# Performance work log

Hardware: AMD Instinct MI355X
Metric: run time of the kernel (lower is better)

## Reference

```python
import jax, jax.numpy as jnp
import numpy as np

B, L, D = 4, 128, 256
EPS = 1e-5

def setup_inputs() -> dict:
    key = jax.random.key(0)
    k1, k2, k3, k4, k5 = jax.random.split(key, 5)
    query = jax.random.normal(k1, (B, L, D), dtype=jnp.float32)
    value = jax.random.normal(k2, (B, L, D), dtype=jnp.float32)
    mask = jax.random.randint(k3, (B, L), 0, 2, dtype=jnp.int32)
    mask = mask.at[:, 0].set(1)  # guarantee at least one valid key per row (avoid all -inf softmax)
    norm3_w = jax.random.normal(k4, (2 * D,), dtype=jnp.float32) * 0.02 + 1.0
    norm3_b = jax.random.normal(k5, (2 * D,), dtype=jnp.float32) * 0.02
    return {"query": query, "value": value, "mask": mask, "norm3_w": norm3_w, "norm3_b": norm3_b}

def reference(query, value, mask, norm3_w, norm3_b):
    # final_queryer[b,i,j,d] = (query[b,i,d] + value[b,j,d]) / 2  -- replaces the eye-matrix expansion
    fq = (query[:, :, None, :] + value[:, None, :, :]) * 0.5          # [B,L,L,D]
    # scores over key axis k against value / query banks
    w = jnp.einsum('bijd,bkd->bijk', fq, value)                        # [B,L,L,L]
    wq = jnp.einsum('bijd,bkd->bijk', fq, query)                       # [B,L,L,L]
    keymask = (mask == 0)[:, None, None, :]                            # [B,1,1,L]
    neg_inf = jnp.float32(-jnp.inf)
    w = jnp.where(keymask, neg_inf, w)
    wq = jnp.where(keymask, neg_inf, wq)
    attn = jax.nn.softmax(w, axis=3)
    attn_q = jax.nn.softmax(wq, axis=3)
    merged = jnp.einsum('bijk,bkd->bijd', attn, value)                 # [B,L,L,D]
    merged_q = jnp.einsum('bijk,bkd->bijd', attn_q, query)             # [B,L,L,D]
    merged = jnp.concatenate([merged, merged_q], axis=-1)              # [B,L,L,2D]
    # LayerNorm over last dim (2D)
    mu = jnp.mean(merged, axis=-1, keepdims=True)
    var = jnp.mean((merged - mu) ** 2, axis=-1, keepdims=True)
    merged = (merged - mu) * jax.lax.rsqrt(var + EPS) * norm3_w + norm3_b
    # re-mask along the i axis
    merged = merged * mask[:, :, None, None].astype(merged.dtype)
    return merged
```

## Files before the change

### kernel.cpp

```cpp
#include <hip/hip_runtime.h>
#include <hip/hip_bf16.h>
#include <stdint.h>

#define BDIM 4
#define LDIM 128
#define DDIM 256
#define CDIM 512
#define EPSLN 1e-5f
#define NE (BDIM * LDIM * LDIM)
#define SROW 516

typedef float f32x4 __attribute__((ext_vector_type(4)));
typedef short s16x8 __attribute__((ext_vector_type(8)));
typedef int i32x4 __attribute__((ext_vector_type(4)));

__device__ __forceinline__ unsigned short f2bf(float f) {
    unsigned u = __builtin_bit_cast(unsigned, f);
    u += 0x7fffu + ((u >> 16) & 1u);
    return (unsigned short)(u >> 16);
}

__device__ __forceinline__ unsigned pk_bf16(float a, float b) {
    union { __hip_bfloat162 h; unsigned u; } cv;
    cv.h = __float22bfloat162_rn(make_float2(a, b));
    return cv.u;
}

__global__ __launch_bounds__(256) void k_transpose(const float* __restrict__ query,
                                                   const float* __restrict__ value,
                                                   float* __restrict__ Qt32,
                                                   float* __restrict__ Vt32,
                                                   unsigned short* __restrict__ Qt16,
                                                   unsigned short* __restrict__ Vt16) {
    __shared__ float tile[32][33];
    const int d0 = blockIdx.x * 32, k0 = blockIdx.y * 32;
    const int b = blockIdx.z & 3, sel = blockIdx.z >> 2;
    const float* src = sel ? query : value;
    float* dst32 = sel ? Qt32 : Vt32;
    unsigned short* dst16 = sel ? Qt16 : Vt16;
    const int tx = threadIdx.x & 31, ty = threadIdx.x >> 5;
#pragma unroll
    for (int jj = 0; jj < 4; ++jj) {
        int r = ty + jj * 8;
        tile[r][tx] = src[((size_t)(b * LDIM + k0 + r)) * DDIM + d0 + tx];
    }
    __syncthreads();
#pragma unroll
    for (int jj = 0; jj < 4; ++jj) {
        int r = ty + jj * 8;
        float v = tile[tx][r];
        size_t o = ((size_t)(b * DDIM + d0 + r)) * LDIM + k0 + tx;
        dst32[o] = v;
        dst16[o] = f2bf(v);
    }
}

__global__ __launch_bounds__(128) void k_gram_e(const float* __restrict__ Qt,
                                                const float* __restrict__ Vt,
                                                const int* __restrict__ mask,
                                                float* __restrict__ Es) {
    const int it = blockIdx.x, which = blockIdx.y, b = blockIdx.z;
    const float* Xt;
    const float* Yt;
    if (which == 0)      { Xt = Qt; Yt = Vt; }
    else if (which == 1) { Xt = Vt; Yt = Vt; }
    else if (which == 2) { Xt = Qt; Yt = Qt; }
    else                 { Xt = Vt; Yt = Qt; }

    const int i0 = it * 16 + ((threadIdx.x >> 5) << 2);
    const int kt = (threadIdx.x & 31) << 2;
    const float* xb = Xt + (size_t)b * DDIM * LDIM + i0;
    const float* yb = Yt + (size_t)b * DDIM * LDIM + kt;

    float acc[4][4] = {};
#pragma unroll 8
    for (int c = 0; c < DDIM; ++c) {
        f32x4 xv = *(const f32x4*)(xb + (size_t)c * LDIM);
        f32x4 yv = *(const f32x4*)(yb + (size_t)c * LDIM);
#pragma unroll
        for (int ii = 0; ii < 4; ++ii)
#pragma unroll
            for (int kk = 0; kk < 4; ++kk)
                acc[ii][kk] += xv[ii] * yv[kk];
    }

    const i32x4 mv = *(const i32x4*)(mask + b * LDIM + kt);
    float* Eg = Es + (size_t)which * NE + (size_t)b * (LDIM * LDIM);
#pragma unroll
    for (int ii = 0; ii < 4; ++ii) {
        float lg[4];
        float mx = -3.0e38f;
#pragma unroll
        for (int kk = 0; kk < 4; ++kk) {
            lg[kk] = 0.5f * acc[ii][kk];
            if (mv[kk] != 0) mx = fmaxf(mx, lg[kk]);
        }
#pragma unroll
        for (int o = 16; o >= 1; o >>= 1) mx = fmaxf(mx, __shfl_xor(mx, o, 64));
        f32x4 r;
#pragma unroll
        for (int kk = 0; kk < 4; ++kk) r[kk] = (mv[kk] != 0) ? __expf(lg[kk] - mx) : 0.0f;
        *(f32x4*)(Eg + (size_t)(i0 + ii) * LDIM + kt) = r;
    }
}

__global__ __launch_bounds__(256, 2) void k_main(const float* __restrict__ E1,
                                                 const unsigned short* __restrict__ Vt16,
                                                 const unsigned short* __restrict__ Qt16,
                                                 const int* __restrict__ mask,
                                                 const float* __restrict__ nw,
                                                 const float* __restrict__ nb,
                                                 float* __restrict__ out) {
    __shared__ __align__(16) char smem[32 * SROW * 4];
    unsigned short (*P_s)[136] = (unsigned short (*)[136])smem;
    unsigned short (*Pq_s)[136] = (unsigned short (*)[136])(smem + 32 * 136 * 2);
    float (*stage)[SROW] = (float (*)[SROW])smem;
    __shared__ float wln[CDIM], bln[CDIM];
    __shared__ float zinv_s[64];
    __shared__ float maskv[32];

    const int tid = threadIdx.x;
    const int i0 = blockIdx.x * 32;
    const int j = blockIdx.y;
    const int b = blockIdx.z;

    const int lane = tid & 63;
    const int q = lane >> 4;
    const int l15 = lane & 15;
    const int wv = tid >> 6;
    const int path = wv >> 1;
    const int nh = wv & 1;

    const float* E2 = E1 + NE;
    const float* E1q = E1 + 2 * NE;
    const float* E2q = E1 + 3 * NE;

    wln[tid] = nw[tid]; wln[tid + 256] = nw[tid + 256];
    bln[tid] = nb[tid]; bln[tid + 256] = nb[tid + 256];
    if (tid < 32) maskv[tid] = (mask[b * LDIM + i0 + tid] != 0) ? 1.0f : 0.0f;

    const unsigned short* bsrc = (path ? Qt16 : Vt16) +
                                 (size_t)b * DDIM * LDIM + (size_t)(nh * 128) * LDIM;
    s16x8 bfr[8][4];
#pragma unroll
    for (int nt = 0; nt < 8; ++nt)
#pragma unroll
        for (int kc = 0; kc < 4; ++kc)
            bfr[nt][kc] = *(const s16x8*)(bsrc + (size_t)(nt * 16 + l15) * LDIM + kc * 32 + q * 8);

    {
        const int m = tid >> 3;
        const int k0 = (tid & 7) * 16;
        const float* e1 = E1 + ((size_t)(b * LDIM + i0 + m)) * LDIM + k0;
        const float* e1q = E1q + ((size_t)(b * LDIM + i0 + m)) * LDIM + k0;
        const float* e2 = E2 + ((size_t)(b * LDIM + j)) * LDIM + k0;
        const float* e2q = E2q + ((size_t)(b * LDIM + j)) * LDIM + k0;
        union { unsigned u32[8]; s16x8 v[2]; } tp, tq;
        float s = 0.f, sq = 0.f;
#pragma unroll
        for (int u4 = 0; u4 < 16; u4 += 4) {
            f32x4 a = *(const f32x4*)(e1 + u4);
            f32x4 c = *(const f32x4*)(e2 + u4);
            f32x4 aq = *(const f32x4*)(e1q + u4);
            f32x4 cq = *(const f32x4*)(e2q + u4);
            float p0 = a[0] * c[0], p1 = a[1] * c[1], p2 = a[2] * c[2], p3 = a[3] * c[3];
            float q0 = aq[0] * cq[0], q1 = aq[1] * cq[1], q2 = aq[2] * cq[2], q3 = aq[3] * cq[3];
            s += (p0 + p1) + (p2 + p3);
            sq += (q0 + q1) + (q2 + q3);
            tp.u32[u4 / 2] = pk_bf16(p0, p1);
            tp.u32[u4 / 2 + 1] = pk_bf16(p2, p3);
            tq.u32[u4 / 2] = pk_bf16(q0, q1);
            tq.u32[u4 / 2 + 1] = pk_bf16(q2, q3);
        }
        *(s16x8*)&P_s[m][k0] = tp.v[0];
        *(s16x8*)&P_s[m][k0 + 8] = tp.v[1];
        *(s16x8*)&Pq_s[m][k0] = tq.v[0];
        *(s16x8*)&Pq_s[m][k0 + 8] = tq.v[1];
        s += __shfl_xor(s, 1, 64); s += __shfl_xor(s, 2, 64); s += __shfl_xor(s, 4, 64);
        sq += __shfl_xor(sq, 1, 64); sq += __shfl_xor(sq, 2, 64); sq += __shfl_xor(sq, 4, 64);
        if ((tid & 7) == 0) { zinv_s[m] = 1.0f / s; zinv_s[32 + m] = 1.0f / sq; }
    }
    __syncthreads();

    f32x4 acc[2][8];
#pragma unroll
    for (int mt = 0; mt < 2; ++mt)
#pragma unroll
        for (int nt = 0; nt < 8; ++nt) acc[mt][nt] = (f32x4){0.f, 0.f, 0.f, 0.f};

    const unsigned short(*As)[136] = path ? Pq_s : P_s;
#pragma unroll
    for (int kc = 0; kc < 4; ++kc) {
        const s16x8 a0 = *(const s16x8*)&As[l15][kc * 32 + q * 8];
        const s16x8 a1 = *(const s16x8*)&As[16 + l15][kc * 32 + q * 8];
#pragma unroll
        for (int nt = 0; nt < 8; ++nt) {
            acc[0][nt] = __builtin_amdgcn_mfma_f32_16x16x32_bf16(a0, bfr[nt][kc], acc[0][nt], 0, 0, 0);
            acc[1][nt] = __builtin_amdgcn_mfma_f32_16x16x32_bf16(a1, bfr[nt][kc], acc[1][nt], 0, 0, 0);
        }
    }
    __syncthreads();

#pragma unroll
    for (int mt = 0; mt < 2; ++mt) {
#pragma unroll
        for (int reg = 0; reg < 4; ++reg) {
            const int row = mt * 16 + q * 4 + reg;
            const float zv = zinv_s[path * 32 + row];
#pragma unroll
            for (int nt = 0; nt < 8; ++nt) {
                const int c = path * 256 + nh * 128 + nt * 16 + l15;
                stage[row][c] = acc[mt][nt][reg] * zv;
            }
        }
    }
    __syncthreads();

    {
        const f32x4 w0 = *(const f32x4*)&wln[lane * 4];
        const f32x4 b0 = *(const f32x4*)&bln[lane * 4];
        const f32x4 w1 = *(const f32x4*)&wln[256 + lane * 4];
        const f32x4 b1 = *(const f32x4*)&bln[256 + lane * 4];
#pragma unroll
        for (int rr = 0; rr < 8; ++rr) {
            const int row = wv * 8 + rr;
            const f32x4 v0 = *(const f32x4*)&stage[row][lane * 4];
            const f32x4 v1 = *(const f32x4*)&stage[row][256 + lane * 4];
            float s1 = (v0[0] + v0[1]) + (v0[2] + v0[3]) + (v1[0] + v1[1]) + (v1[2] + v1[3]);
            float s2 = (v0[0] * v0[0] + v0[1] * v0[1]) + (v0[2] * v0[2] + v0[3] * v0[3]) +
                       (v1[0] * v1[0] + v1[1] * v1[1]) + (v1[2] * v1[2] + v1[3] * v1[3]);
#pragma unroll
            for (int o = 1; o <= 32; o <<= 1) {
                s1 += __shfl_xor(s1, o, 64);
                s2 += __shfl_xor(s2, o, 64);
            }
            const float mean = s1 * (1.0f / 512.0f);
            const float var = s2 * (1.0f / 512.0f) - mean * mean;
            const float rstd = rsqrtf(var + EPSLN);
            const float mf = maskv[row];
            float* orow = out + (((size_t)(b * LDIM + i0 + row)) * LDIM + j) * CDIM;
            f32x4 o0, o1;
#pragma unroll
            for (int u = 0; u < 4; ++u) {
                o0[u] = ((v0[u] - mean) * rstd * w0[u] + b0[u]) * mf;
                o1[u] = ((v1[u] - mean) * rstd * w1[u] + b1[u]) * mf;
            }
            *(f32x4*)&orow[lane * 4] = o0;
            *(f32x4*)&orow[256 + lane * 4] = o1;
        }
    }
}

extern "C" void kernel_launch(void* const* d_in, const int* in_sizes, int n_in,
                              void* d_out, int out_size, void* d_ws, size_t ws_size,
                              hipStream_t stream) {
    const float* query = (const float*)d_in[0];
    const float* value = (const float*)d_in[1];
    const int* mask = (const int*)d_in[2];
    const float* nw = (const float*)d_in[3];
    const float* nb = (const float*)d_in[4];
    float* out = (float*)d_out;

    char* ws = (char*)d_ws;
    const size_t NT = (size_t)BDIM * DDIM * LDIM;

    float* Es = (float*)ws;
    unsigned short* Vt16 = (unsigned short*)(ws + 4 * (size_t)NE * 4);
    unsigned short* Qt16 = Vt16 + NT;
    float* Vt32 = (float*)(ws + 4 * (size_t)NE * 4 + 2 * NT * 2);
    float* Qt32 = Vt32 + NT;

    k_transpose<<<dim3(8, 4, 8), 256, 0, stream>>>(query, value, Qt32, Vt32, Qt16, Vt16);
    k_gram_e<<<dim3(8, 4, 4), 128, 0, stream>>>(Qt32, Vt32, mask, Es);
    k_main<<<dim3(4, 128, 4), 256, 0, stream>>>(Es, Vt16, Qt16, mask, nw, nb, out);
}
```

Baseline: 238.3 us.

## Process four j per block and fuse LayerNorm into MFMA registers

Each k_main block now handles four j values instead of one. This amortizes the B-fragment register loads, the LN weight loads and the E1 row loads across four outputs, and cuts the grid size by four. The LayerNorm no longer stages the full 32x512 tile in shared memory. Row sums are reduced directly from the MFMA accumulators with shuffles plus a small double-buffered cross-wave buffer, and outputs are written straight from registers. The trade-off is that output stores become scalar strided writes (16 lanes contiguous) instead of 128-bit vector stores, and there is less block-level parallelism.

```diff
diff --git a/kernel.cpp b/kernel.cpp
--- a/kernel.cpp
+++ b/kernel.cpp
@@ -8,7 +8,7 @@
 #define CDIM 512
 #define EPSLN 1e-5f
 #define NE (BDIM * LDIM * LDIM)
-#define SROW 516
+#define JT 4
 
 typedef float f32x4 __attribute__((ext_vector_type(4)));
 typedef short s16x8 __attribute__((ext_vector_type(8)));
@@ -111,17 +111,15 @@
                                                  const float* __restrict__ nw,
                                                  const float* __restrict__ nb,
                                                  float* __restrict__ out) {
-    __shared__ __align__(16) char smem[32 * SROW * 4];
-    unsigned short (*P_s)[136] = (unsigned short (*)[136])smem;
-    unsigned short (*Pq_s)[136] = (unsigned short (*)[136])(smem + 32 * 136 * 2);
-    float (*stage)[SROW] = (float (*)[SROW])smem;
+    __shared__ __align__(16) unsigned short P_s[JT][2][32][136];
     __shared__ float wln[CDIM], bln[CDIM];
-    __shared__ float zinv_s[64];
+    __shared__ float zinv_s[JT][2][32];
+    __shared__ __align__(16) float red[2][32][4][2];
     __shared__ float maskv[32];
 
     const int tid = threadIdx.x;
     const int i0 = blockIdx.x * 32;
-    const int j = blockIdx.y;
+    const int j0 = blockIdx.y * JT;
     const int b = blockIdx.z;
 
     const int lane = tid & 63;
@@ -153,101 +151,105 @@
         const int k0 = (tid & 7) * 16;
         const float* e1 = E1 + ((size_t)(b * LDIM + i0 + m)) * LDIM + k0;
         const float* e1q = E1q + ((size_t)(b * LDIM + i0 + m)) * LDIM + k0;
-        const float* e2 = E2 + ((size_t)(b * LDIM + j)) * LDIM + k0;
-        const float* e2q = E2q + ((size_t)(b * LDIM + j)) * LDIM + k0;
-        union { unsigned u32[8]; s16x8 v[2]; } tp, tq;
-        float s = 0.f, sq = 0.f;
+        const float* e2 = E2 + ((size_t)(b * LDIM + j0)) * LDIM + k0;
+        const float* e2q = E2q + ((size_t)(b * LDIM + j0)) * LDIM + k0;
+        float s[JT] = {}, sq[JT] = {};
 #pragma unroll
         for (int u4 = 0; u4 < 16; u4 += 4) {
-            f32x4 a = *(const f32x4*)(e1 + u4);
-            f32x4 c = *(const f32x4*)(e2 + u4);
-            f32x4 aq = *(const f32x4*)(e1q + u4);
-            f32x4 cq = *(const f32x4*)(e2q + u4);
-            float p0 = a[0] * c[0], p1 = a[1] * c[1], p2 = a[2] * c[2], p3 = a[3] * c[3];
-            float q0 = aq[0] * cq[0], q1 = aq[1] * cq[1], q2 = aq[2] * cq[2], q3 = aq[3] * cq[3];
-            s += (p0 + p1) + (p2 + p3);
-            sq += (q0 + q1) + (q2 + q3);
-            tp.u32[u4 / 2] = pk_bf16(p0, p1);
-            tp.u32[u4 / 2 + 1] = pk_bf16(p2, p3);
-            tq.u32[u4 / 2] = pk_bf16(q0, q1);
-            tq.u32[u4 / 2 + 1] = pk_bf16(q2, q3);
-        }
-        *(s16x8*)&P_s[m][k0] = tp.v[0];
-        *(s16x8*)&P_s[m][k0 + 8] = tp.v[1];
-        *(s16x8*)&Pq_s[m][k0] = tq.v[0];
-        *(s16x8*)&Pq_s[m][k0 + 8] = tq.v[1];
-        s += __shfl_xor(s, 1, 64); s += __shfl_xor(s, 2, 64); s += __shfl_xor(s, 4, 64);
-        sq += __shfl_xor(sq, 1, 64); sq += __shfl_xor(sq, 2, 64); sq += __shfl_xor(sq, 4, 64);
-        if ((tid & 7) == 0) { zinv_s[m] = 1.0f / s; zinv_s[32 + m] = 1.0f / sq; }
+            const f32x4 a = *(const f32x4*)(e1 + u4);
+            const f32x4 aq = *(const f32x4*)(e1q + u4);
+#pragma unroll
+            for (int jj = 0; jj < JT; ++jj) {
+                const f32x4 c = *(const f32x4*)(e2 + jj * LDIM + u4);
+                const f32x4 cq = *(const f32x4*)(e2q + jj * LDIM + u4);
+                const float p0 = a[0] * c[0], p1 = a[1] * c[1];
+                const float p2 = a[2] * c[2], p3 = a[3] * c[3];
+                const float r0 = aq[0] * cq[0], r1 = aq[1] * cq[1];
+                const float r2 = aq[2] * cq[2], r3 = aq[3] * cq[3];
+                s[jj] += (p0 + p1) + (p2 + p3);
+                sq[jj] += (r0 + r1) + (r2 + r3);
+                uint2 wp; wp.x = pk_bf16(p0, p1); wp.y = pk_bf16(p2, p3);
+                uint2 wq2; wq2.x = pk_bf16(r0, r1); wq2.y = pk_bf16(r2, r3);
+                *(uint2*)&P_s[jj][0][m][k0 + u4] = wp;
+                *(uint2*)&P_s[jj][1][m][k0 + u4] = wq2;
+            }
+        }
+#pragma unroll
+        for (int jj = 0; jj < JT; ++jj) {
+            float s_ = s[jj], sq_ = sq[jj];
+            s_ += __shfl_xor(s_, 1, 64); s_ += __shfl_xor(s_, 2, 64); s_ += __shfl_xor(s_, 4, 64);
+            sq_ += __shfl_xor(sq_, 1, 64); sq_ += __shfl_xor(sq_, 2, 64); sq_ += __shfl_xor(sq_, 4, 64);
+            if ((tid & 7) == 0) { zinv_s[jj][0][m] = 1.0f / s_; zinv_s[jj][1][m] = 1.0f / sq_; }
+        }
     }
     __syncthreads();
 
-    f32x4 acc[2][8];
-#pragma unroll
-    for (int mt = 0; mt < 2; ++mt)
-#pragma unroll
-        for (int nt = 0; nt < 8; ++nt) acc[mt][nt] = (f32x4){0.f, 0.f, 0.f, 0.f};
-
-    const unsigned short(*As)[136] = path ? Pq_s : P_s;
-#pragma unroll
-    for (int kc = 0; kc < 4; ++kc) {
-        const s16x8 a0 = *(const s16x8*)&As[l15][kc * 32 + q * 8];
-        const s16x8 a1 = *(const s16x8*)&As[16 + l15][kc * 32 + q * 8];
-#pragma unroll
-        for (int nt = 0; nt < 8; ++nt) {
-            acc[0][nt] = __builtin_amdgcn_mfma_f32_16x16x32_bf16(a0, bfr[nt][kc], acc[0][nt], 0, 0, 0);
-            acc[1][nt] = __builtin_amdgcn_mfma_f32_16x16x32_bf16(a1, bfr[nt][kc], acc[1][nt], 0, 0, 0);
-        }
-    }
-    __syncthreads();
-
-#pragma unroll
-    for (int mt = 0; mt < 2; ++mt) {
-#pragma unroll
-        for (int reg = 0; reg < 4; ++reg) {
-            const int row = mt * 16 + q * 4 + reg;
-            const float zv = zinv_s[path * 32 + row];
+    const int c0 = path * 256 + nh * 128 + l15;
+    float wreg[8], breg[8];
+#pragma unroll
+    for (int nt = 0; nt < 8; ++nt) { wreg[nt] = wln[c0 + nt * 16]; breg[nt] = bln[c0 + nt * 16]; }
+
+#pragma unroll 1
+    for (int jj = 0; jj < JT; ++jj) {
+        f32x4 acc[2][8];
+#pragma unroll
+        for (int mt = 0; mt < 2; ++mt)
+#pragma unroll
+            for (int nt = 0; nt < 8; ++nt) acc[mt][nt] = (f32x4){0.f, 0.f, 0.f, 0.f};
+
+        const unsigned short(*As)[136] = P_s[jj][path];
+#pragma unroll
+        for (int kc = 0; kc < 4; ++kc) {
+            const s16x8 a0 = *(const s16x8*)&As[l15][kc * 32 + q * 8];
+            const s16x8 a1 = *(const s16x8*)&As[16 + l15][kc * 32 + q * 8];
 #pragma unroll
             for (int nt = 0; nt < 8; ++nt) {
-                const int c = path * 256 + nh * 128 + nt * 16 + l15;
-                stage[row][c] = acc[mt][nt][reg] * zv;
-            }
-        }
-    }
-    __syncthreads();
-
-    {
-        const f32x4 w0 = *(const f32x4*)&wln[lane * 4];
-        const f32x4 b0 = *(const f32x4*)&bln[lane * 4];
-        const f32x4 w1 = *(const f32x4*)&wln[256 + lane * 4];
-        const f32x4 b1 = *(const f32x4*)&bln[256 + lane * 4];
-#pragma unroll
-        for (int rr = 0; rr < 8; ++rr) {
-            const int row = wv * 8 + rr;
-            const f32x4 v0 = *(const f32x4*)&stage[row][lane * 4];
-            const f32x4 v1 = *(const f32x4*)&stage[row][256 + lane * 4];
-            float s1 = (v0[0] + v0[1]) + (v0[2] + v0[3]) + (v1[0] + v1[1]) + (v1[2] + v1[3]);
-            float s2 = (v0[0] * v0[0] + v0[1] * v0[1]) + (v0[2] * v0[2] + v0[3] * v0[3]) +
-                       (v1[0] * v1[0] + v1[1] * v1[1]) + (v1[2] * v1[2] + v1[3] * v1[3]);
-#pragma unroll
-            for (int o = 1; o <= 32; o <<= 1) {
-                s1 += __shfl_xor(s1, o, 64);
-                s2 += __shfl_xor(s2, o, 64);
-            }
-            const float mean = s1 * (1.0f / 512.0f);
-            const float var = s2 * (1.0f / 512.0f) - mean * mean;
-            const float rstd = rsqrtf(var + EPSLN);
-            const float mf = maskv[row];
-            float* orow = out + (((size_t)(b * LDIM + i0 + row)) * LDIM + j) * CDIM;
-            f32x4 o0, o1;
-#pragma unroll
-            for (int u = 0; u < 4; ++u) {
-                o0[u] = ((v0[u] - mean) * rstd * w0[u] + b0[u]) * mf;
-                o1[u] = ((v1[u] - mean) * rstd * w1[u] + b1[u]) * mf;
-            }
-            *(f32x4*)&orow[lane * 4] = o0;
-            *(f32x4*)&orow[256 + lane * 4] = o1;
-        }
+                acc[0][nt] = __builtin_amdgcn_mfma_f32_16x16x32_bf16(a0, bfr[nt][kc], acc[0][nt], 0, 0, 0);
+                acc[1][nt] = __builtin_amdgcn_mfma_f32_16x16x32_bf16(a1, bfr[nt][kc], acc[1][nt], 0, 0, 0);
+            }
+        }
+
+        const int rb = jj & 1;
+#pragma unroll
+        for (int mt = 0; mt < 2; ++mt)
+#pragma unroll
+            for (int reg = 0; reg < 4; ++reg) {
+                const int row = mt * 16 + q * 4 + reg;
+                const float zv = zinv_s[jj][path][row];
+                float s1 = 0.f, s2 = 0.f;
+#pragma unroll
+                for (int nt = 0; nt < 8; ++nt) {
+                    const float v = acc[mt][nt][reg] * zv;
+                    acc[mt][nt][reg] = v;
+                    s1 += v; s2 += v * v;
+                }
+#pragma unroll
+                for (int o = 1; o <= 8; o <<= 1) {
+                    s1 += __shfl_xor(s1, o, 64);
+                    s2 += __shfl_xor(s2, o, 64);
+                }
+                if (l15 == 0) { red[rb][row][wv][0] = s1; red[rb][row][wv][1] = s2; }
+            }
+        __syncthreads();
+
+#pragma unroll
+        for (int mt = 0; mt < 2; ++mt)
+#pragma unroll
+            for (int reg = 0; reg < 4; ++reg) {
+                const int row = mt * 16 + q * 4 + reg;
+                const f32x4 r0 = *(const f32x4*)&red[rb][row][0][0];
+                const f32x4 r1 = *(const f32x4*)&red[rb][row][2][0];
+                const float s1t = (r0[0] + r0[2]) + (r1[0] + r1[2]);
+                const float s2t = (r0[1] + r0[3]) + (r1[1] + r1[3]);
+                const float mean = s1t * (1.0f / 512.0f);
+                const float var = s2t * (1.0f / 512.0f) - mean * mean;
+                const float rstd = rsqrtf(var + EPSLN);
+                const float mf = maskv[row];
+                float* orow = out + (((size_t)(b * LDIM + i0 + row)) * LDIM + (j0 + jj)) * CDIM + c0;
+#pragma unroll
+                for (int nt = 0; nt < 8; ++nt)
+                    orow[nt * 16] = ((acc[mt][nt][reg] - mean) * rstd * wreg[nt] + breg[nt]) * mf;
+            }
     }
 }
 
@@ -272,5 +274,5 @@
 
     k_transpose<<<dim3(8, 4, 8), 256, 0, stream>>>(query, value, Qt32, Vt32, Qt16, Vt16);
     k_gram_e<<<dim3(8, 4, 4), 128, 0, stream>>>(Qt32, Vt32, mask, Es);
-    k_main<<<dim3(4, 128, 4), 256, 0, stream>>>(Es, Vt16, Qt16, mask, nw, nb, out);
-}
+    k_main<<<dim3(4, 32, 4), 256, 0, stream>>>(Es, Vt16, Qt16, mask, nw, nb, out);
+}
```

Result: slower. 253.3 us (+6.3%).

## Fuse transpose and gram-softmax kernels into one prep kernel using LDS tiles

Applied to the files above, without the earlier changes.

Merges the transpose and Gram/exp kernels into a single launch. The Gram computation now reads query/value directly in row-major form, staged through shared memory, instead of going through fp32 transposed copies. This removes the fp32 transpose writes, one kernel launch, and a dependency stage. The cost is more shared memory per block and Es stores that are no longer vectorised.

```diff
diff --git a/kernel.cpp b/kernel.cpp
--- a/kernel.cpp
+++ b/kernel.cpp
@@ -26,65 +26,93 @@
     return cv.u;
 }
 
-__global__ __launch_bounds__(256) void k_transpose(const float* __restrict__ query,
-                                                   const float* __restrict__ value,
-                                                   float* __restrict__ Qt32,
-                                                   float* __restrict__ Vt32,
-                                                   unsigned short* __restrict__ Qt16,
-                                                   unsigned short* __restrict__ Vt16) {
-    __shared__ float tile[32][33];
-    const int d0 = blockIdx.x * 32, k0 = blockIdx.y * 32;
-    const int b = blockIdx.z & 3, sel = blockIdx.z >> 2;
-    const float* src = sel ? query : value;
-    float* dst32 = sel ? Qt32 : Vt32;
-    unsigned short* dst16 = sel ? Qt16 : Vt16;
-    const int tx = threadIdx.x & 31, ty = threadIdx.x >> 5;
-#pragma unroll
-    for (int jj = 0; jj < 4; ++jj) {
-        int r = ty + jj * 8;
-        tile[r][tx] = src[((size_t)(b * LDIM + k0 + r)) * DDIM + d0 + tx];
-    }
-    __syncthreads();
-#pragma unroll
-    for (int jj = 0; jj < 4; ++jj) {
-        int r = ty + jj * 8;
-        float v = tile[tx][r];
-        size_t o = ((size_t)(b * DDIM + d0 + r)) * LDIM + k0 + tx;
-        dst32[o] = v;
-        dst16[o] = f2bf(v);
-    }
-}
-
-__global__ __launch_bounds__(128) void k_gram_e(const float* __restrict__ Qt,
-                                                const float* __restrict__ Vt,
-                                                const int* __restrict__ mask,
-                                                float* __restrict__ Es) {
-    const int it = blockIdx.x, which = blockIdx.y, b = blockIdx.z;
-    const float* Xt;
-    const float* Yt;
-    if (which == 0)      { Xt = Qt; Yt = Vt; }
-    else if (which == 1) { Xt = Vt; Yt = Vt; }
-    else if (which == 2) { Xt = Qt; Yt = Qt; }
-    else                 { Xt = Vt; Yt = Qt; }
-
-    const int i0 = it * 16 + ((threadIdx.x >> 5) << 2);
-    const int kt = (threadIdx.x & 31) << 2;
-    const float* xb = Xt + (size_t)b * DDIM * LDIM + i0;
-    const float* yb = Yt + (size_t)b * DDIM * LDIM + kt;
+__global__ __launch_bounds__(128) void k_prep(const float* __restrict__ query,
+                                              const float* __restrict__ value,
+                                              const int* __restrict__ mask,
+                                              float* __restrict__ Es,
+                                              unsigned short* __restrict__ Qt16,
+                                              unsigned short* __restrict__ Vt16) {
+    __shared__ __align__(16) char smem[16 * 260 * 4 + 128 * 68 * 4];
+    float (*X_s)[260] = (float (*)[260])smem;
+    float (*Y_s)[68] = (float (*)[68])(smem + 16 * 260 * 4);
+    float (*tile)[33] = (float (*)[33])smem;
+
+    const int t = threadIdx.x;
+
+    if (blockIdx.z >= 4) {
+        const int z2 = blockIdx.z - 4;
+        const int b = z2 & 3, sel = z2 >> 2;
+        const int d0 = blockIdx.x * 32, k0 = blockIdx.y * 32;
+        const float* src = sel ? query : value;
+        unsigned short* dst16 = sel ? Qt16 : Vt16;
+        const int tx = t & 31, ty = t >> 5;
+#pragma unroll
+        for (int jj = 0; jj < 8; ++jj) {
+            int r = ty + jj * 4;
+            tile[r][tx] = src[((size_t)(b * LDIM + k0 + r)) * DDIM + d0 + tx];
+        }
+        __syncthreads();
+#pragma unroll
+        for (int jj = 0; jj < 8; ++jj) {
+            int r = ty + jj * 4;
+            size_t o = ((size_t)(b * DDIM + d0 + r)) * LDIM + k0 + tx;
+            dst16[o] = f2bf(tile[tx][r]);
+        }
+        return;
+    }
+
+    const int b = blockIdx.z, which = blockIdx.y, it = blockIdx.x;
+    const float* X = (which == 0 || which == 2) ? query : value;
+    const float* Y = (which <= 1) ? value : query;
+    const float* Xb = X + (size_t)b * LDIM * DDIM;
+    const float* Yb = Y + (size_t)b * LDIM * DDIM;
+
+    const int i0 = it * 16;
+    const int iq = (t >> 5) << 2;
+    const int kl = t & 31;
+
+#pragma unroll
+    for (int u = 0; u < 8; ++u) {
+        int ch = u * 128 + t;
+        int row = ch >> 6;
+        int cc = (ch & 63) << 2;
+        *(f32x4*)&X_s[row][cc] = *(const f32x4*)(Xb + (size_t)(i0 + row) * DDIM + cc);
+    }
 
     float acc[4][4] = {};
-#pragma unroll 8
-    for (int c = 0; c < DDIM; ++c) {
-        f32x4 xv = *(const f32x4*)(xb + (size_t)c * LDIM);
-        f32x4 yv = *(const f32x4*)(yb + (size_t)c * LDIM);
-#pragma unroll
-        for (int ii = 0; ii < 4; ++ii)
-#pragma unroll
-            for (int kk = 0; kk < 4; ++kk)
-                acc[ii][kk] += xv[ii] * yv[kk];
-    }
-
-    const i32x4 mv = *(const i32x4*)(mask + b * LDIM + kt);
+#pragma unroll 1
+    for (int ct = 0; ct < 4; ++ct) {
+#pragma unroll
+        for (int u = 0; u < 16; ++u) {
+            int ch = u * 128 + t;
+            int row = ch >> 4;
+            int cc = (ch & 15) << 2;
+            *(f32x4*)&Y_s[row][cc] = *(const f32x4*)(Yb + (size_t)row * DDIM + ct * 64 + cc);
+        }
+        __syncthreads();
+#pragma unroll
+        for (int u = 0; u < 16; ++u) {
+            const int c = u * 4;
+            f32x4 xv[4], yv[4];
+#pragma unroll
+            for (int ii = 0; ii < 4; ++ii) xv[ii] = *(const f32x4*)&X_s[iq + ii][ct * 64 + c];
+#pragma unroll
+            for (int kk = 0; kk < 4; ++kk) yv[kk] = *(const f32x4*)&Y_s[kl + 32 * kk][c];
+#pragma unroll
+            for (int ii = 0; ii < 4; ++ii)
+#pragma unroll
+                for (int kk = 0; kk < 4; ++kk)
+#pragma unroll
+                    for (int e = 0; e < 4; ++e)
+                        acc[ii][kk] += xv[ii][e] * yv[kk][e];
+        }
+        __syncthreads();
+    }
+
+    int mk[4];
+#pragma unroll
+    for (int kk = 0; kk < 4; ++kk) mk[kk] = mask[b * LDIM + kl + 32 * kk];
+
     float* Eg = Es + (size_t)which * NE + (size_t)b * (LDIM * LDIM);
 #pragma unroll
     for (int ii = 0; ii < 4; ++ii) {
@@ -93,14 +121,14 @@
 #pragma unroll
         for (int kk = 0; kk < 4; ++kk) {
             lg[kk] = 0.5f * acc[ii][kk];
-            if (mv[kk] != 0) mx = fmaxf(mx, lg[kk]);
+            if (mk[kk] != 0) mx = fmaxf(mx, lg[kk]);
         }
 #pragma unroll
         for (int o = 16; o >= 1; o >>= 1) mx = fmaxf(mx, __shfl_xor(mx, o, 64));
-        f32x4 r;
-#pragma unroll
-        for (int kk = 0; kk < 4; ++kk) r[kk] = (mv[kk] != 0) ? __expf(lg[kk] - mx) : 0.0f;
-        *(f32x4*)(Eg + (size_t)(i0 + ii) * LDIM + kt) = r;
+#pragma unroll
+        for (int kk = 0; kk < 4; ++kk)
+            Eg[(size_t)(i0 + iq + ii) * LDIM + kl + 32 * kk] =
+                (mk[kk] != 0) ? __expf(lg[kk] - mx) : 0.0f;
     }
 }
 
@@ -267,10 +295,7 @@
     float* Es = (float*)ws;
     unsigned short* Vt16 = (unsigned short*)(ws + 4 * (size_t)NE * 4);
     unsigned short* Qt16 = Vt16 + NT;
-    float* Vt32 = (float*)(ws + 4 * (size_t)NE * 4 + 2 * NT * 2);
-    float* Qt32 = Vt32 + NT;
-
-    k_transpose<<<dim3(8, 4, 8), 256, 0, stream>>>(query, value, Qt32, Vt32, Qt16, Vt16);
-    k_gram_e<<<dim3(8, 4, 4), 128, 0, stream>>>(Qt32, Vt32, mask, Es);
+
+    k_prep<<<dim3(8, 4, 12), 128, 0, stream>>>(query, value, mask, Es, Qt16, Vt16);
     k_main<<<dim3(4, 128, 4), 256, 0, stream>>>(Es, Vt16, Qt16, mask, nw, nb, out);
 }
```

After: 193.2 us. 1.23x faster.
